# Kernel tuning notes

Measured on AMD Instinct MI355X. Metric: run time of the kernel, lower is better.

Reference implementation:

```python
import jax, jax.numpy as jnp
import numpy as np

DECAY = 0.99


def setup_inputs() -> dict:
    key = jax.random.key(0)
    k1, k2, k3 = jax.random.split(key, 3)
    B, D, H, W = 16, 128, 32, 32
    K = 8192
    z_e = jax.random.normal(k1, (B, D, H, W), dtype=jnp.float32)
    codebook = jax.random.normal(k2, (K, D), dtype=jnp.float32)
    ema_count = jnp.ones((K,), dtype=jnp.float32)
    ema_weight = codebook  # buffer initialized as codebook.clone()
    return {"z_e": z_e, "codebook": codebook, "ema_count": ema_count, "ema_weight": ema_weight}


def reference(z_e, codebook, ema_count, ema_weight):
    B, D, H, W = z_e.shape
    K = codebook.shape[0]
    # (B,D,H,W) -> (N,D)
    z_flat = z_e.transpose(0, 2, 3, 1).reshape(-1, D)
    # squared L2 distances: ||z||^2 - 2 z.C^T + ||C||^2  -> (N,K)
    dist = (
        jnp.sum(z_flat * z_flat, axis=1, keepdims=True)
        - 2.0 * (z_flat @ codebook.T)
        + jnp.sum(codebook * codebook, axis=1)[None, :]
    )
    indices = jnp.argmin(dist, axis=1)  # (N,)
    z_q = codebook[indices].reshape(B, H, W, D).transpose(0, 3, 1, 2)
    # EMA codebook update (training path, no grad)
    counts = jax.ops.segment_sum(jnp.ones_like(indices, dtype=jnp.float32), indices, num_segments=K)
    dw = jax.ops.segment_sum(z_flat, indices, num_segments=K)  # (K,D)
    new_count = ema_count * DECAY + (1.0 - DECAY) * counts
    new_weight = ema_weight * DECAY + (1.0 - DECAY) * dw
    new_codebook = new_weight / jnp.maximum(new_count, 1.0)[:, None]
    # straight-through estimator
    z_q_st = z_e + jax.lax.stop_gradient(z_q - z_e)
    return (z_q_st, indices.reshape(B, H, W), new_codebook, new_count, new_weight)
```

## Files before the change

### kernel.cpp

```cpp
#include <hip/hip_runtime.h>

#define D 128
#define HW 1024
#define NROWS 16384
#define K 8192
#define NU 32

#define OUT0 0
#define OUT1 2097152
#define OUT2 2113536
#define OUT3 3162112
#define OUT4 3170304

typedef __attribute__((ext_vector_type(8))) _Float16 half8;
typedef __attribute__((ext_vector_type(16))) float f32x16;
typedef unsigned short u16;
typedef unsigned long long u64;

__device__ __forceinline__ void gld16(const u16* gsrc, u16* ldst) {
    __builtin_amdgcn_global_load_lds(
        (const __attribute__((address_space(1))) unsigned int*)gsrc,
        (__attribute__((address_space(3))) unsigned int*)ldst,
        16, 0, 0);
}

__global__ __launch_bounds__(256) void k_prep(const float* __restrict__ cb,
                                              const float* __restrict__ z_e,
                                              u16* __restrict__ Bg,
                                              float* __restrict__ cnorm,
                                              u16* __restrict__ Ah, u16* __restrict__ Al,
                                              u64* __restrict__ packed,
                                              float* __restrict__ counts,
                                              float* __restrict__ dw) {
    const int tid = threadIdx.x;
    if (blockIdx.x < 512) {
        int kk = tid & 15;
        int k = blockIdx.x * 16 + (tid >> 4);
        const float* src = cb + (size_t)k * D + kk * 8;
        half8 h, l;
        float s = 0.f;
#pragma unroll
        for (int j = 0; j < 8; ++j) {
            float v = src[j];
            s += v * v;
            _Float16 hv = (_Float16)v;
            _Float16 lv = (_Float16)(v - (float)hv);
            h[j] = hv;
            l[j] = lv;
        }
        int g = k >> 5, col = k & 31;
        size_t offH = (size_t)g * 8192 + ((size_t)kk * 32 + col) * 8;
        *(half8*)((_Float16*)Bg + offH) = h;
        *(half8*)((_Float16*)Bg + offH + 4096) = l;
#pragma unroll
        for (int off = 8; off > 0; off >>= 1) s += __shfl_down(s, off);
        if (kk == 0) cnorm[k] = s;
        float4 z4 = {0.f, 0.f, 0.f, 0.f};
        size_t zi = ((size_t)blockIdx.x * 256 + tid) * 8;
        *(float4*)(dw + zi) = z4;
        *(float4*)(dw + zi + 4) = z4;
    } else {
        int gid = (blockIdx.x - 512) * 256 + tid;
        int n  = gid & (NROWS - 1);
        int kk = gid >> 14;
        int b = n >> 10, hw = n & 1023;
        const float* src = z_e + ((size_t)b * D + kk * 8) * HW + hw;
        half8 h, l;
#pragma unroll
        for (int j = 0; j < 8; ++j) {
            float v = src[(size_t)j * HW];
            _Float16 hv = (_Float16)v;
            _Float16 lv = (_Float16)(v - (float)hv);
            h[j] = hv;
            l[j] = lv;
        }
        int rg = n >> 7, band = (n >> 5) & 3, row = n & 31;
        size_t off = (((((size_t)rg * 4 + band) * 8 + (kk >> 1)) * 2 + (kk & 1)) * 32 + row) * 8;
        *(half8*)(Ah + off) = h;
        *(half8*)(Al + off) = l;
        if (kk == 0) {
            packed[n] = ~0ull;
            if (n < K) counts[n] = 0.f;
        }
    }
}

__global__ __launch_bounds__(256, 2) void k_argmin_mfma(
        const u16* __restrict__ Ahg, const u16* __restrict__ Alg,
        const u16* __restrict__ Bg,
        const float* __restrict__ cnorm, u64* __restrict__ packed) {
    __shared__ u16 lds[2][8192];

    const int tid = threadIdx.x;
    const int ln  = tid & 63;
    const int l31 = ln & 31;
    const int lh  = ln >> 5;
    const int wy  = tid >> 6;

    const int bid = blockIdx.x;
    const int ks_ = bid & 7;
    const int rg  = bid >> 3;

    const int k0 = ks_ * 1024;
    const int g0 = k0 >> 5;
    const int band = rg * 4 + wy;

    half8 Ah[8], Al[8];
#pragma unroll
    for (int ks = 0; ks < 8; ++ks) {
        size_t off = ((((size_t)band * 8 + ks) * 2 + lh) * 32 + l31) * 8;
        Ah[ks] = *(const half8*)((const _Float16*)Ahg + off);
        Al[ks] = *(const half8*)((const _Float16*)Alg + off);
    }

    {
        const u16* src = Bg + (size_t)g0 * 8192;
#pragma unroll
        for (int r = 0; r < 4; ++r)
            gld16(src + ((size_t)r * 256 + tid) * 8, lds[0] + (r * 256 + tid) * 8);
    }
    asm volatile("s_waitcnt vmcnt(0)" ::: "memory");
    asm volatile("s_barrier" ::: "memory");

    float minv[16];
    int   mini[16];
#pragma unroll
    for (int r = 0; r < 16; ++r) { minv[r] = INFINITY; mini[r] = 0; }

#pragma unroll 1
    for (int u = 0; u < NU; ++u) {
        const u16* buf = lds[u & 1];
        const int c0 = k0 + u * 32 + l31;

        float cn0 = cnorm[c0];

        if (u + 1 < NU) {
            const u16* src = Bg + (size_t)(g0 + u + 1) * 8192;
            u16* dst = lds[(u + 1) & 1];
#pragma unroll
            for (int r = 0; r < 4; ++r)
                gld16(src + ((size_t)r * 256 + tid) * 8, dst + (r * 256 + tid) * 8);
            asm volatile("s_waitcnt vmcnt(5)" ::: "memory");
        } else {
            asm volatile("s_waitcnt vmcnt(0)" ::: "memory");
        }
        asm volatile("s_barrier" ::: "memory");

        const _Float16* bh = (const _Float16*)buf;
        const _Float16* bl = bh + 4096;

        half8 b[16];
#pragma unroll
        for (int ks = 0; ks < 8; ++ks)
            b[ks] = *(const half8*)(bl + ((ks * 2 + lh) * 32 + l31) * 8);
#pragma unroll
        for (int ks = 0; ks < 8; ++ks)
            b[8 + ks] = *(const half8*)(bh + ((ks * 2 + lh) * 32 + l31) * 8);

        f32x16 acc = {};
        __builtin_amdgcn_s_setprio(1);
#pragma unroll
        for (int ks = 0; ks < 8; ++ks)
            acc = __builtin_amdgcn_mfma_f32_32x32x16_f16(Ah[ks], b[ks], acc, 0, 0, 0);
#pragma unroll
        for (int ks = 0; ks < 8; ++ks) {
            acc = __builtin_amdgcn_mfma_f32_32x32x16_f16(Ah[ks], b[8 + ks], acc, 0, 0, 0);
            acc = __builtin_amdgcn_mfma_f32_32x32x16_f16(Al[ks], b[8 + ks], acc, 0, 0, 0);
        }
        __builtin_amdgcn_s_setprio(0);

#pragma unroll
        for (int r = 0; r < 16; ++r) {
            float d0 = fmaf(-2.0f, acc[r], cn0);
            bool p = d0 < minv[r];
            minv[r] = p ? d0 : minv[r];
            mini[r] = p ? c0 : mini[r];
        }
        asm volatile("s_barrier" ::: "memory");
    }

#pragma unroll
    for (int r = 0; r < 16; ++r) {
        float v = minv[r];
        int ix = mini[r];
#pragma unroll
        for (int off = 1; off < 32; off <<= 1) {
            float v2 = __shfl_xor(v, off);
            int i2 = __shfl_xor(ix, off);
            if (v2 < v || (v2 == v && i2 < ix)) { v = v2; ix = i2; }
        }
        if (l31 == 0) {
            int row = band * 32 + 4 * lh + (r & 3) + 8 * (r >> 2);
            unsigned int uenc = __float_as_uint(v);
            uenc = (uenc & 0x80000000u) ? ~uenc : (uenc | 0x80000000u);
            u64 pk = ((u64)uenc << 13) | (u64)(unsigned)ix;
            atomicMin(&packed[row], pk);
        }
    }
}

__global__ __launch_bounds__(256) void k_epilogue(const float* __restrict__ z_e,
                                                  const float* __restrict__ cb,
                                                  const u64* __restrict__ packed,
                                                  float* __restrict__ out0,
                                                  float* __restrict__ out1,
                                                  float* __restrict__ counts,
                                                  float* __restrict__ dw) {
    __shared__ int idxS[64];
    const int tid = threadIdx.x;
    const int n0 = blockIdx.x * 64;
    const int bb = n0 >> 10, p0 = n0 & 1023;

    if (tid < 64) {
        int ix = (int)(packed[n0 + tid] & 0x1FFFull);
        idxS[tid] = ix;
        out1[n0 + tid] = (float)ix;
        atomicAdd(&counts[ix], 1.0f);
    }
    __syncthreads();

    const float* zb = z_e + (size_t)bb * (D * HW) + p0;
    float* ob = out0 + (size_t)bb * (D * HW) + p0;

    for (int i = tid; i < 64 * D; i += 256) {
        int d = i >> 6, r = i & 63;
        float z = zb[(size_t)d * HW + r];
        float c = cb[(size_t)idxS[r] * D + d];
        ob[(size_t)d * HW + r] = z + (c - z);
    }
    for (int i = tid; i < 64 * D; i += 256) {
        int r = i >> 7, d = i & 127;
        atomicAdd(&dw[(size_t)idxS[r] * D + d], zb[(size_t)d * HW + r]);
    }
}

__global__ __launch_bounds__(256) void k_final(const float* __restrict__ ema_count,
                                               const float* __restrict__ ema_weight,
                                               float* __restrict__ out2,
                                               float* __restrict__ out3,
                                               float* __restrict__ out4) {
    int gid = blockIdx.x * 256 + threadIdx.x;
    int k = gid >> 7, d = gid & 127;
    float cnt_raw = out3[k];
    float dw_raw = out4[gid];
    __syncthreads();
    float nc = 0.99f * ema_count[k] + 0.01f * cnt_raw;
    float nw = 0.99f * ema_weight[gid] + 0.01f * dw_raw;
    out4[gid] = nw;
    out2[gid] = nw / fmaxf(nc, 1.0f);
    if (d == 0) out3[k] = nc;
}

extern "C" void kernel_launch(void* const* d_in, const int* in_sizes, int n_in,
                              void* d_out, int out_size, void* d_ws, size_t ws_size,
                              hipStream_t stream) {
    const float* z_e        = (const float*)d_in[0];
    const float* cb         = (const float*)d_in[1];
    const float* ema_count  = (const float*)d_in[2];
    const float* ema_weight = (const float*)d_in[3];
    float* out = (float*)d_out;

    float* cnorm = (float*)d_ws;
    u64* packed = (u64*)((char*)d_ws + K * 4);

    u16* Ahg = (u16*)(out + OUT0);
    u16* Alg = Ahg + (size_t)NROWS * D;
    u16* Bg  = (u16*)(out + OUT2);

    k_prep       <<<1536,          256, 0, stream>>>(cb, z_e, Bg, cnorm, Ahg, Alg,
                                                     packed, out + OUT3, out + OUT4);
    k_argmin_mfma<<<1024,          256, 0, stream>>>(Ahg, Alg, Bg, cnorm, packed);
    k_epilogue   <<<NROWS / 64,    256, 0, stream>>>(z_e, cb, packed,
                                                     out + OUT0, out + OUT1,
                                                     out + OUT3, out + OUT4);
    k_final      <<<(K * D) / 256, 256, 0, stream>>>(ema_count, ema_weight,
                                                     out + OUT2, out + OUT3, out + OUT4);
}
```

Baseline: 218.1 us.

## Software-pipeline argmin epilogue with MFMA using ping-pong accumulators and raise occupancy

The codebook loop is unrolled by two and uses two accumulators. The distance/argmin update for the previous tile is interleaved with the MFMA chain of the current tile. B fragments are loaded from LDS one at a time instead of into a 16-entry register array. Launch bounds go from 2 to 3 blocks per CU, and the block-index mapping is changed so that neighbouring blocks share a codebook slice. Together these aim to hide the VALU epilogue behind the matrix core and improve latency hiding, at the risk of register pressure or spills under the tighter occupancy bound.

```diff
diff --git a/kernel.cpp b/kernel.cpp
--- a/kernel.cpp
+++ b/kernel.cpp
@@ -85,7 +85,7 @@
     }
 }
 
-__global__ __launch_bounds__(256, 2) void k_argmin_mfma(
+__global__ __launch_bounds__(256, 3) void k_argmin_mfma(
         const u16* __restrict__ Ahg, const u16* __restrict__ Alg,
         const u16* __restrict__ Bg,
         const float* __restrict__ cnorm, u64* __restrict__ packed) {
@@ -98,8 +98,8 @@
     const int wy  = tid >> 6;
 
     const int bid = blockIdx.x;
-    const int ks_ = bid & 7;
-    const int rg  = bid >> 3;
+    const int ks_ = (bid >> 3) & 7;
+    const int rg  = (bid & 7) * 16 + (bid >> 6);
 
     const int k0 = ks_ * 1024;
     const int g0 = k0 >> 5;
@@ -127,56 +127,99 @@
 #pragma unroll
     for (int r = 0; r < 16; ++r) { minv[r] = INFINITY; mini[r] = 0; }
 
+    f32x16 accA = {}, accB = {};
+    float cnA = INFINITY, cnB = INFINITY;
+    int   cA = 0, cB = 0;
+
 #pragma unroll 1
-    for (int u = 0; u < NU; ++u) {
-        const u16* buf = lds[u & 1];
-        const int c0 = k0 + u * 32 + l31;
-
-        float cn0 = cnorm[c0];
-
-        if (u + 1 < NU) {
+    for (int u = 0; u < NU; u += 2) {
+        {
+            cA = k0 + u * 32 + l31;
+            float cn_new = cnorm[cA];
             const u16* src = Bg + (size_t)(g0 + u + 1) * 8192;
-            u16* dst = lds[(u + 1) & 1];
 #pragma unroll
             for (int r = 0; r < 4; ++r)
-                gld16(src + ((size_t)r * 256 + tid) * 8, dst + (r * 256 + tid) * 8);
+                gld16(src + ((size_t)r * 256 + tid) * 8, lds[1] + (r * 256 + tid) * 8);
             asm volatile("s_waitcnt vmcnt(5)" ::: "memory");
-        } else {
-            asm volatile("s_waitcnt vmcnt(0)" ::: "memory");
-        }
-        asm volatile("s_barrier" ::: "memory");
-
-        const _Float16* bh = (const _Float16*)buf;
-        const _Float16* bl = bh + 4096;
-
-        half8 b[16];
-#pragma unroll
-        for (int ks = 0; ks < 8; ++ks)
-            b[ks] = *(const half8*)(bl + ((ks * 2 + lh) * 32 + l31) * 8);
-#pragma unroll
-        for (int ks = 0; ks < 8; ++ks)
-            b[8 + ks] = *(const half8*)(bh + ((ks * 2 + lh) * 32 + l31) * 8);
-
-        f32x16 acc = {};
-        __builtin_amdgcn_s_setprio(1);
-#pragma unroll
-        for (int ks = 0; ks < 8; ++ks)
-            acc = __builtin_amdgcn_mfma_f32_32x32x16_f16(Ah[ks], b[ks], acc, 0, 0, 0);
-#pragma unroll
-        for (int ks = 0; ks < 8; ++ks) {
-            acc = __builtin_amdgcn_mfma_f32_32x32x16_f16(Ah[ks], b[8 + ks], acc, 0, 0, 0);
-            acc = __builtin_amdgcn_mfma_f32_32x32x16_f16(Al[ks], b[8 + ks], acc, 0, 0, 0);
-        }
-        __builtin_amdgcn_s_setprio(0);
-
-#pragma unroll
-        for (int r = 0; r < 16; ++r) {
-            float d0 = fmaf(-2.0f, acc[r], cn0);
-            bool p = d0 < minv[r];
-            minv[r] = p ? d0 : minv[r];
-            mini[r] = p ? c0 : mini[r];
-        }
-        asm volatile("s_barrier" ::: "memory");
+            asm volatile("s_barrier" ::: "memory");
+
+            const _Float16* bh = (const _Float16*)lds[0];
+            const _Float16* bl = bh + 4096;
+
+            accA = f32x16{};
+            __builtin_amdgcn_s_setprio(1);
+#pragma unroll
+            for (int ks = 0; ks < 8; ++ks) {
+                half8 b = *(const half8*)(bl + ((ks * 2 + lh) * 32 + l31) * 8);
+                accA = __builtin_amdgcn_mfma_f32_32x32x16_f16(Ah[ks], b, accA, 0, 0, 0);
+            }
+#pragma unroll
+            for (int ks = 0; ks < 8; ++ks) {
+                half8 b = *(const half8*)(bh + ((ks * 2 + lh) * 32 + l31) * 8);
+                accA = __builtin_amdgcn_mfma_f32_32x32x16_f16(Ah[ks], b, accA, 0, 0, 0);
+                accA = __builtin_amdgcn_mfma_f32_32x32x16_f16(Al[ks], b, accA, 0, 0, 0);
+                const int r0 = ks * 2, r1 = r0 + 1;
+                float d0 = fmaf(-2.0f, accB[r0], cnB);
+                float d1 = fmaf(-2.0f, accB[r1], cnB);
+                bool p0 = d0 < minv[r0];
+                bool p1 = d1 < minv[r1];
+                minv[r0] = p0 ? d0 : minv[r0];  mini[r0] = p0 ? cB : mini[r0];
+                minv[r1] = p1 ? d1 : minv[r1];  mini[r1] = p1 ? cB : mini[r1];
+            }
+            __builtin_amdgcn_s_setprio(0);
+            cnA = cn_new;
+            asm volatile("s_barrier" ::: "memory");
+        }
+
+        {
+            cB = k0 + (u + 1) * 32 + l31;
+            float cn_new = cnorm[cB];
+            if (u + 2 < NU) {
+                const u16* src = Bg + (size_t)(g0 + u + 2) * 8192;
+#pragma unroll
+                for (int r = 0; r < 4; ++r)
+                    gld16(src + ((size_t)r * 256 + tid) * 8, lds[0] + (r * 256 + tid) * 8);
+                asm volatile("s_waitcnt vmcnt(5)" ::: "memory");
+            } else {
+                asm volatile("s_waitcnt vmcnt(0)" ::: "memory");
+            }
+            asm volatile("s_barrier" ::: "memory");
+
+            const _Float16* bh = (const _Float16*)lds[1];
+            const _Float16* bl = bh + 4096;
+
+            accB = f32x16{};
+            __builtin_amdgcn_s_setprio(1);
+#pragma unroll
+            for (int ks = 0; ks < 8; ++ks) {
+                half8 b = *(const half8*)(bl + ((ks * 2 + lh) * 32 + l31) * 8);
+                accB = __builtin_amdgcn_mfma_f32_32x32x16_f16(Ah[ks], b, accB, 0, 0, 0);
+            }
+#pragma unroll
+            for (int ks = 0; ks < 8; ++ks) {
+                half8 b = *(const half8*)(bh + ((ks * 2 + lh) * 32 + l31) * 8);
+                accB = __builtin_amdgcn_mfma_f32_32x32x16_f16(Ah[ks], b, accB, 0, 0, 0);
+                accB = __builtin_amdgcn_mfma_f32_32x32x16_f16(Al[ks], b, accB, 0, 0, 0);
+                const int r0 = ks * 2, r1 = r0 + 1;
+                float d0 = fmaf(-2.0f, accA[r0], cnA);
+                float d1 = fmaf(-2.0f, accA[r1], cnA);
+                bool p0 = d0 < minv[r0];
+                bool p1 = d1 < minv[r1];
+                minv[r0] = p0 ? d0 : minv[r0];  mini[r0] = p0 ? cA : mini[r0];
+                minv[r1] = p1 ? d1 : minv[r1];  mini[r1] = p1 ? cA : mini[r1];
+            }
+            __builtin_amdgcn_s_setprio(0);
+            cnB = cn_new;
+            asm volatile("s_barrier" ::: "memory");
+        }
+    }
+
+#pragma unroll
+    for (int r = 0; r < 16; ++r) {
+        float d0 = fmaf(-2.0f, accB[r], cnB);
+        bool p = d0 < minv[r];
+        minv[r] = p ? d0 : minv[r];
+        mini[r] = p ? cB : mini[r];
     }
 
 #pragma unroll
```

Result: faster. 211.9 us (-2.8%).
